# Kernel tuning notes

Measured on AMD Instinct MI355X. Metric: run time of the kernel, lower is better.

The kernel has to match this reference:

```python
import jax, jax.numpy as jnp
import numpy as np

A = -0.75  # torch bicubic kernel parameter

def _cubic_weights(t):
    # torch get_cubic_upsample_coefficients, a = -0.75; t = frac in [0, 1)
    def k1(x):  # |x| <= 1
        return ((A + 2.0) * x - (A + 3.0)) * x * x + 1.0
    def k2(x):  # 1 < |x| < 2
        return ((A * x - 5.0 * A) * x + 8.0 * A) * x - 4.0 * A
    return (k2(t + 1.0), k1(t), k1(1.0 - t), k2(2.0 - t))

def _reflect_clip(idx, size):
    # reflection padding about border pixel centers (align_corners=True), then clip
    span = size - 1
    i = jnp.abs(idx)
    i = jnp.mod(i, 2 * span)
    i = jnp.where(i > span, 2 * span - i, i)
    return jnp.clip(i, 0, span)

def _grid_sample_bicubic(img, gx, gy):
    # img: (C,H,W); gx,gy: (H,W) normalized coords (grid_sample convention)
    C, H, W = img.shape
    ix = (gx + 1.0) * 0.5 * (W - 1)  # align_corners=True unnormalize
    iy = (gy + 1.0) * 0.5 * (H - 1)
    x0 = jnp.floor(ix)
    y0 = jnp.floor(iy)
    wx = _cubic_weights(ix - x0)
    wy = _cubic_weights(iy - y0)
    x0i = x0.astype(jnp.int32)
    y0i = y0.astype(jnp.int32)
    out = jnp.zeros((C, H, W), img.dtype)
    for dy in range(4):
        yi = _reflect_clip(y0i + (dy - 1), H)
        row = jnp.zeros((C, H, W), img.dtype)
        for dx in range(4):
            xi = _reflect_clip(x0i + (dx - 1), W)
            row = row + wx[dx] * img[:, yi, xi]  # (C,H,W) gather
        out = out + wy[dy] * row
    return out

def setup_inputs() -> dict:
    key = jax.random.key(0)
    kx, kr, kc = jax.random.split(key, 3)
    B, C, H, W = 16, 8, 512, 512
    x = jax.random.normal(kx, (B, C, H, W), dtype=jnp.float32)
    rates = jnp.array([0.25, 0.5, 0.75], dtype=jnp.float32)
    idx = jax.random.randint(kr, (B,), 0, rates.shape[0])
    downsampling_rate = rates[idx]
    # center = 2*rand - 1, as in sample_downsampling_parameters
    center = 2.0 * jax.random.uniform(kc, (B, 2), dtype=jnp.float32) - 1.0
    return {"x": x, "downsampling_rate": downsampling_rate, "center": center}

def reference(x, downsampling_rate, center):
    B, C, H, W = x.shape
    # grid as built by get_downsampling_grid (module requires H == W)
    gx = (2.0 / W) * jnp.arange(W, dtype=x.dtype) - 1.0  # width coord  (channel 0)
    gy = (2.0 / H) * jnp.arange(H, dtype=x.dtype) - 1.0  # height coord (channel 1)
    gx = jnp.broadcast_to(gx[None, :], (H, W))
    gy = jnp.broadcast_to(gy[:, None], (H, W))
    r = downsampling_rate[:, None, None]                 # (B,1,1)
    cx = center[:, 0][:, None, None]
    cy = center[:, 1][:, None, None]
    Gx = (gx[None] - cx) / r + cx                        # (B,H,W)
    Gy = (gy[None] - cy) / r + cy
    return jax.vmap(_grid_sample_bicubic)(x, Gx, Gy)
```

## Files before the change

### kernel.cpp

```cpp
#include <hip/hip_runtime.h>
#include <string.h>

#define AA (-0.75f)

__device__ __forceinline__ float k1f(float x) {
    return ((AA + 2.0f) * x - (AA + 3.0f)) * x * x + 1.0f;
}
__device__ __forceinline__ float k2f(float x) {
    return ((AA * x - 5.0f * AA) * x + 8.0f * AA) * x - 4.0f * AA;
}

__device__ __forceinline__ int reflect_clip(int idx, int size) {
    int span = size - 1;
    int i = idx < 0 ? -idx : idx;
    i = i % (2 * span);
    if (i > span) i = 2 * span - i;
    return i;
}

__device__ __forceinline__ int swz(int a) { return a ^ ((a >> 5) & 31); }

__global__ __launch_bounds__(256, 4)
void pds5_kernel(const float* __restrict__ x,
                 const float* __restrict__ rate,
                 const float* __restrict__ center,
                 float* __restrict__ out)
{
    constexpr int C = 8, H = 512, W = 512;

    const int orig = blockIdx.x;
    const int id = (orig & 7) * 1024 + (orig >> 3);
    const int b = id >> 9;
    const int h = id & (H - 1);

    const float r  = rate[b];
    const float cx = center[2 * b + 0];
    const float cy = center[2 * b + 1];
    const float inv_r = 1.0f / r;
    const int t = threadIdx.x;

    const float gy = 0.00390625f * (float)h - 1.0f;
    const float Gy = (gy - cy) * inv_r + cy;
    const float iy = (Gy + 1.0f) * 0.5f * 511.0f;
    const float y0 = floorf(iy);
    const float ty = iy - y0;
    const int   y0i = (int)y0;
    const float wy0 = k2f(ty + 1.0f);
    const float wy1 = k1f(ty);
    const float wy2 = k1f(1.0f - ty);
    const float wy3 = k2f(2.0f - ty);
    const int ro0 = reflect_clip(y0i - 1, H) * W;
    const int ro1 = reflect_clip(y0i    , H) * W;
    const int ro2 = reflect_clip(y0i + 1, H) * W;
    const int ro3 = reflect_clip(y0i + 2, H) * W;

    const float* imgb = x + (size_t)b * C * H * W;
    const int cc4 = (t & 127) << 2;
    const int ch0 = (t >> 7);
    const float* base0 = imgb + (size_t)(ch0 + 0) * (H * W) + cc4;
    const float* base1 = imgb + (size_t)(ch0 + 2) * (H * W) + cc4;
    const float* base2 = imgb + (size_t)(ch0 + 4) * (H * W) + cc4;
    const float* base3 = imgb + (size_t)(ch0 + 6) * (H * W) + cc4;

    float4 p00 = *(const float4*)(base0 + ro0);
    float4 p01 = *(const float4*)(base0 + ro1);
    float4 p02 = *(const float4*)(base0 + ro2);
    float4 p03 = *(const float4*)(base0 + ro3);
    float4 p10 = *(const float4*)(base1 + ro0);
    float4 p11 = *(const float4*)(base1 + ro1);
    float4 p12 = *(const float4*)(base1 + ro2);
    float4 p13 = *(const float4*)(base1 + ro3);
    float4 p20 = *(const float4*)(base2 + ro0);
    float4 p21 = *(const float4*)(base2 + ro1);
    float4 p22 = *(const float4*)(base2 + ro2);
    float4 p23 = *(const float4*)(base2 + ro3);
    float4 p30 = *(const float4*)(base3 + ro0);
    float4 p31 = *(const float4*)(base3 + ro1);
    float4 p32 = *(const float4*)(base3 + ro2);
    float4 p33 = *(const float4*)(base3 + ro3);
    asm volatile("" ::: "memory");

    int   sA0, sA1, sA2, sA3, sB0, sB1, sB2, sB3;
    float wxA0, wxA1, wxA2, wxA3, wxB0, wxB1, wxB2, wxB3;
    {
        const int w = 2 * t;
        const float gx = 0.00390625f * (float)w - 1.0f;
        const float Gx = (gx - cx) * inv_r + cx;
        const float ix = (Gx + 1.0f) * 0.5f * 511.0f;
        const float x0 = floorf(ix);
        const float tx = ix - x0;
        const int x0i = (int)x0;
        wxA0 = k2f(tx + 1.0f); wxA1 = k1f(tx);
        wxA2 = k1f(1.0f - tx); wxA3 = k2f(2.0f - tx);
        sA0 = swz(reflect_clip(x0i - 1, W)); sA1 = swz(reflect_clip(x0i,     W));
        sA2 = swz(reflect_clip(x0i + 1, W)); sA3 = swz(reflect_clip(x0i + 2, W));
    }
    {
        const int w = 2 * t + 1;
        const float gx = 0.00390625f * (float)w - 1.0f;
        const float Gx = (gx - cx) * inv_r + cx;
        const float ix = (Gx + 1.0f) * 0.5f * 511.0f;
        const float x0 = floorf(ix);
        const float tx = ix - x0;
        const int x0i = (int)x0;
        wxB0 = k2f(tx + 1.0f); wxB1 = k1f(tx);
        wxB2 = k1f(1.0f - tx); wxB3 = k2f(2.0f - tx);
        sB0 = swz(reflect_clip(x0i - 1, W)); sB1 = swz(reflect_clip(x0i,     W));
        sB2 = swz(reflect_clip(x0i + 1, W)); sB3 = swz(reflect_clip(x0i + 2, W));
    }

    __shared__ float tmp[C][W];

    {
        const int v    = (cc4 >> 5) & 31;
        const int base = cc4 ^ (v & ~3);
        const int p    = v & 3;
        const bool q1 = (p & 1) != 0;
        const bool q2 = (p & 2) != 0;
#define COMB1(cc, a0, a1, a2, a3)                                          \
        {                                                                  \
            float e0 = wy0 * a0.x + wy1 * a1.x + wy2 * a2.x + wy3 * a3.x;  \
            float e1 = wy0 * a0.y + wy1 * a1.y + wy2 * a2.y + wy3 * a3.y;  \
            float e2 = wy0 * a0.z + wy1 * a1.z + wy2 * a2.z + wy3 * a3.z;  \
            float e3 = wy0 * a0.w + wy1 * a1.w + wy2 * a2.w + wy3 * a3.w;  \
            float t0 = q1 ? e1 : e0;                                       \
            float t1 = q1 ? e0 : e1;                                       \
            float t2 = q1 ? e3 : e2;                                       \
            float t3 = q1 ? e2 : e3;                                       \
            float u0 = q2 ? t2 : t0;                                       \
            float u1 = q2 ? t3 : t1;                                       \
            float u2 = q2 ? t0 : t2;                                       \
            float u3 = q2 ? t1 : t3;                                       \
            *(float4*)&tmp[cc][base] = make_float4(u0, u1, u2, u3);        \
        }
        COMB1(ch0 + 0, p00, p01, p02, p03);
        COMB1(ch0 + 2, p10, p11, p12, p13);
        COMB1(ch0 + 4, p20, p21, p22, p23);
        COMB1(ch0 + 6, p30, p31, p32, p33);
#undef COMB1
    }
    __syncthreads();

    float* obase = out + ((size_t)b * C * H + h) * W + 2 * t;
    #pragma unroll
    for (int c = 0; c < C; ++c) {
        const float* tr = tmp[c];
        const float s0 = wxA0 * tr[sA0] + wxA1 * tr[sA1]
                       + wxA2 * tr[sA2] + wxA3 * tr[sA3];
        const float s1 = wxB0 * tr[sB0] + wxB1 * tr[sB1]
                       + wxB2 * tr[sB2] + wxB3 * tr[sB3];
        float2 v2 = make_float2(s0, s1);
        double dv;
        memcpy(&dv, &v2, 8);
        __builtin_nontemporal_store(dv, (double*)(obase + (size_t)c * (H * W)));
    }
}

extern "C" void kernel_launch(void* const* d_in, const int* in_sizes, int n_in,
                              void* d_out, int out_size, void* d_ws, size_t ws_size,
                              hipStream_t stream) {
    const float* x      = (const float*)d_in[0];
    const float* rate   = (const float*)d_in[1];
    const float* center = (const float*)d_in[2];
    float* out          = (float*)d_out;

    constexpr int B = 16, H = 512;
    dim3 grid(B * H);
    dim3 block(256);
    pds5_kernel<<<grid, block, 0, stream>>>(x, rate, center, out);
}
```

Before: 56.84 us.

## Split each output row across two 128-thread blocks of four channels each

Each block now handles one output row for four channels instead of all eight, using 128 threads and twice as many blocks. Each thread computes four output columns and writes them with one 16-byte nontemporal store instead of two columns with an 8-byte store. Shared memory per block is halved and occupancy hints change. The horizontal tap indices and weights are now computed once per block per half, so that work is done twice per row, and each thread carries more registers.

Measured after the change: 57.46 us. No clear change (+1.1%).

```diff
diff --git a/kernel.cpp b/kernel.cpp
--- a/kernel.cpp
+++ b/kernel.cpp
@@ -1,5 +1,4 @@
 #include <hip/hip_runtime.h>
-#include <string.h>
 
 #define AA (-0.75f)
 
@@ -20,24 +19,29 @@
 
 __device__ __forceinline__ int swz(int a) { return a ^ ((a >> 5) & 31); }
 
-__global__ __launch_bounds__(256, 4)
-void pds5_kernel(const float* __restrict__ x,
+typedef float f32x4 __attribute__((ext_vector_type(4)));
+
+__global__ __launch_bounds__(128, 6)
+void pds7_kernel(const float* __restrict__ x,
                  const float* __restrict__ rate,
                  const float* __restrict__ center,
                  float* __restrict__ out)
 {
-    constexpr int C = 8, H = 512, W = 512;
+    constexpr int C = 8, H = 512, W = 512, HW = H * W;
 
     const int orig = blockIdx.x;
-    const int id = (orig & 7) * 1024 + (orig >> 3);
-    const int b = id >> 9;
-    const int h = id & (H - 1);
+    const int id   = (orig & 7) * 2048 + (orig >> 3);
+    const int b    = id >> 10;
+    const int rem  = id & 1023;
+    const int h    = rem >> 1;
+    const int half = rem & 1;
+    const int ch0  = half * 4;
+    const int t    = threadIdx.x;
 
     const float r  = rate[b];
     const float cx = center[2 * b + 0];
     const float cy = center[2 * b + 1];
     const float inv_r = 1.0f / r;
-    const int t = threadIdx.x;
 
     const float gy = 0.00390625f * (float)h - 1.0f;
     const float Gy = (gy - cy) * inv_r + cy;
@@ -54,13 +58,12 @@
     const int ro2 = reflect_clip(y0i + 1, H) * W;
     const int ro3 = reflect_clip(y0i + 2, H) * W;
 
-    const float* imgb = x + (size_t)b * C * H * W;
-    const int cc4 = (t & 127) << 2;
-    const int ch0 = (t >> 7);
-    const float* base0 = imgb + (size_t)(ch0 + 0) * (H * W) + cc4;
-    const float* base1 = imgb + (size_t)(ch0 + 2) * (H * W) + cc4;
-    const float* base2 = imgb + (size_t)(ch0 + 4) * (H * W) + cc4;
-    const float* base3 = imgb + (size_t)(ch0 + 6) * (H * W) + cc4;
+    const float* imgb = x + (size_t)b * C * HW;
+    const int cc4 = t << 2;
+    const float* base0 = imgb + (size_t)(ch0 + 0) * HW + cc4;
+    const float* base1 = imgb + (size_t)(ch0 + 1) * HW + cc4;
+    const float* base2 = imgb + (size_t)(ch0 + 2) * HW + cc4;
+    const float* base3 = imgb + (size_t)(ch0 + 3) * HW + cc4;
 
     float4 p00 = *(const float4*)(base0 + ro0);
     float4 p01 = *(const float4*)(base0 + ro1);
@@ -80,36 +83,28 @@
     float4 p33 = *(const float4*)(base3 + ro3);
     asm volatile("" ::: "memory");
 
-    int   sA0, sA1, sA2, sA3, sB0, sB1, sB2, sB3;
-    float wxA0, wxA1, wxA2, wxA3, wxB0, wxB1, wxB2, wxB3;
-    {
-        const int w = 2 * t;
-        const float gx = 0.00390625f * (float)w - 1.0f;
-        const float Gx = (gx - cx) * inv_r + cx;
-        const float ix = (Gx + 1.0f) * 0.5f * 511.0f;
-        const float x0 = floorf(ix);
-        const float tx = ix - x0;
-        const int x0i = (int)x0;
-        wxA0 = k2f(tx + 1.0f); wxA1 = k1f(tx);
-        wxA2 = k1f(1.0f - tx); wxA3 = k2f(2.0f - tx);
-        sA0 = swz(reflect_clip(x0i - 1, W)); sA1 = swz(reflect_clip(x0i,     W));
-        sA2 = swz(reflect_clip(x0i + 1, W)); sA3 = swz(reflect_clip(x0i + 2, W));
+    int   s00,s01,s02,s03, s10,s11,s12,s13, s20,s21,s22,s23, s30,s31,s32,s33;
+    float w00,w01,w02,w03, w10,w11,w12,w13, w20,w21,w22,w23, w30,w31,w32,w33;
+#define XTAP(wcol, S0,S1,S2,S3, W0,W1,W2,W3)                               \
+    {                                                                      \
+        const float gx = 0.00390625f * (float)(wcol) - 1.0f;               \
+        const float Gx = (gx - cx) * inv_r + cx;                           \
+        const float ix = (Gx + 1.0f) * 0.5f * 511.0f;                      \
+        const float x0 = floorf(ix);                                       \
+        const float tx = ix - x0;                                          \
+        const int x0i = (int)x0;                                           \
+        W0 = k2f(tx + 1.0f); W1 = k1f(tx);                                 \
+        W2 = k1f(1.0f - tx); W3 = k2f(2.0f - tx);                          \
+        S0 = swz(reflect_clip(x0i - 1, W)); S1 = swz(reflect_clip(x0i,     W)); \
+        S2 = swz(reflect_clip(x0i + 1, W)); S3 = swz(reflect_clip(x0i + 2, W)); \
     }
-    {
-        const int w = 2 * t + 1;
-        const float gx = 0.00390625f * (float)w - 1.0f;
-        const float Gx = (gx - cx) * inv_r + cx;
-        const float ix = (Gx + 1.0f) * 0.5f * 511.0f;
-        const float x0 = floorf(ix);
-        const float tx = ix - x0;
-        const int x0i = (int)x0;
-        wxB0 = k2f(tx + 1.0f); wxB1 = k1f(tx);
-        wxB2 = k1f(1.0f - tx); wxB3 = k2f(2.0f - tx);
-        sB0 = swz(reflect_clip(x0i - 1, W)); sB1 = swz(reflect_clip(x0i,     W));
-        sB2 = swz(reflect_clip(x0i + 1, W)); sB3 = swz(reflect_clip(x0i + 2, W));
-    }
+    XTAP(4 * t + 0, s00,s01,s02,s03, w00,w01,w02,w03);
+    XTAP(4 * t + 1, s10,s11,s12,s13, w10,w11,w12,w13);
+    XTAP(4 * t + 2, s20,s21,s22,s23, w20,w21,w22,w23);
+    XTAP(4 * t + 3, s30,s31,s32,s33, w30,w31,w32,w33);
+#undef XTAP
 
-    __shared__ float tmp[C][W];
+    __shared__ float tmp[4][W];
 
     {
         const int v    = (cc4 >> 5) & 31;
@@ -117,7 +112,7 @@
         const int p    = v & 3;
         const bool q1 = (p & 1) != 0;
         const bool q2 = (p & 2) != 0;
-#define COMB1(cc, a0, a1, a2, a3)                                          \
+#define COMB1(k, a0, a1, a2, a3)                                           \
         {                                                                  \
             float e0 = wy0 * a0.x + wy1 * a1.x + wy2 * a2.x + wy3 * a3.x;  \
             float e1 = wy0 * a0.y + wy1 * a1.y + wy2 * a2.y + wy3 * a3.y;  \
@@ -131,28 +126,26 @@
             float u1 = q2 ? t3 : t1;                                       \
             float u2 = q2 ? t0 : t2;                                       \
             float u3 = q2 ? t1 : t3;                                       \
-            *(float4*)&tmp[cc][base] = make_float4(u0, u1, u2, u3);        \
+            *(float4*)&tmp[k][base] = make_float4(u0, u1, u2, u3);         \
         }
-        COMB1(ch0 + 0, p00, p01, p02, p03);
-        COMB1(ch0 + 2, p10, p11, p12, p13);
-        COMB1(ch0 + 4, p20, p21, p22, p23);
-        COMB1(ch0 + 6, p30, p31, p32, p33);
+        COMB1(0, p00, p01, p02, p03);
+        COMB1(1, p10, p11, p12, p13);
+        COMB1(2, p20, p21, p22, p23);
+        COMB1(3, p30, p31, p32, p33);
 #undef COMB1
     }
     __syncthreads();
 
-    float* obase = out + ((size_t)b * C * H + h) * W + 2 * t;
+    float* ob = out + (((size_t)(b * C + ch0)) * H + h) * W + (t << 2);
     #pragma unroll
-    for (int c = 0; c < C; ++c) {
+    for (int c = 0; c < 4; ++c) {
         const float* tr = tmp[c];
-        const float s0 = wxA0 * tr[sA0] + wxA1 * tr[sA1]
-                       + wxA2 * tr[sA2] + wxA3 * tr[sA3];
-        const float s1 = wxB0 * tr[sB0] + wxB1 * tr[sB1]
-                       + wxB2 * tr[sB2] + wxB3 * tr[sB3];
-        float2 v2 = make_float2(s0, s1);
-        double dv;
-        memcpy(&dv, &v2, 8);
-        __builtin_nontemporal_store(dv, (double*)(obase + (size_t)c * (H * W)));
+        const float o0 = w00 * tr[s00] + w01 * tr[s01] + w02 * tr[s02] + w03 * tr[s03];
+        const float o1 = w10 * tr[s10] + w11 * tr[s11] + w12 * tr[s12] + w13 * tr[s13];
+        const float o2 = w20 * tr[s20] + w21 * tr[s21] + w22 * tr[s22] + w23 * tr[s23];
+        const float o3 = w30 * tr[s30] + w31 * tr[s31] + w32 * tr[s32] + w33 * tr[s33];
+        f32x4 v = {o0, o1, o2, o3};
+        __builtin_nontemporal_store(v, (f32x4*)(ob + (size_t)c * HW));
     }
 }
 
@@ -165,7 +158,7 @@
     float* out          = (float*)d_out;
 
     constexpr int B = 16, H = 512;
-    dim3 grid(B * H);
-    dim3 block(256);
-    pds5_kernel<<<grid, block, 0, stream>>>(x, rate, center, out);
+    dim3 grid(B * H * 2);
+    dim3 block(128);
+    pds7_kernel<<<grid, block, 0, stream>>>(x, rate, center, out);
 }
```
